# Optimization experiments

Measured on AMD Instinct MI355X. Metric: run time of the kernel, lower is better.

## Reference

```python
import jax, jax.numpy as jnp
import numpy as np

NEG_INF = -1.0e9  # matches torch code's masked fill value


def setup_inputs() -> dict:
    key = jax.random.key(0)
    k1, k2, k3, k4 = jax.random.split(key, 4)
    n, q, s, d, v = 8, 4096, 4096, 64, 64
    return {
        "queries_nqd": jax.random.normal(k1, (n, q, d), dtype=jnp.float32),
        "keys_nsd": jax.random.normal(k2, (n, s, d), dtype=jnp.float32),
        "values_nsv": jax.random.normal(k3, (n, s, v), dtype=jnp.float32),
        "attention_mask_nqs": jax.random.randint(k4, (n, q, s), 0, 2).astype(jnp.bool_),
    }


def reference(queries_nqd, keys_nsd, values_nsv, attention_mask_nqs):
    d = queries_nqd.shape[-1]
    scale = 1.0 / jnp.sqrt(jnp.asarray(d, dtype=queries_nqd.dtype))
    # [n,q,s] = [n,q,d] @ [n,d,s]
    scores_nqs = jnp.einsum("nqd,nsd->nqs", queries_nqd, keys_nsd) * scale
    scores_nqs = jnp.where(attention_mask_nqs, scores_nqs, jnp.asarray(NEG_INF, scores_nqs.dtype))
    probs_nqs = jax.nn.softmax(scores_nqs, axis=-1)
    # dropout p=0.0 (eval) -> identity
    return jnp.einsum("nqs,nsv->nqv", probs_nqs, values_nsv)
```

## Files before the change

kernel.cpp:

```cpp
#include <hip/hip_runtime.h>
#include <hip/hip_bf16.h>


#define NHEADS 8
#define QLEN   4096
#define SLEN   4096
#define DDIM   64
#define VDIM   64
#define SBLK   64
#define QBLK   64
#define NWAVES 4
#define NCHUNK (SLEN / SBLK)

typedef __bf16          bf16x4 __attribute__((ext_vector_type(4)));
typedef __bf16          bf16x8 __attribute__((ext_vector_type(8)));
typedef float           f32x4  __attribute__((ext_vector_type(4)));
typedef unsigned int    u32x4  __attribute__((ext_vector_type(4)));
typedef unsigned short  u16x4  __attribute__((ext_vector_type(4)));

#define KSWZ(s) (((s) & 7) << 4)
#define VSWZ(v) ((((v) >> 2) & 7) << 4)

__device__ __forceinline__ int detect_mfmt(const unsigned char* __restrict__ M) {
  const int lane = threadIdx.x & 63;
  u32x4 w = *((const u32x4*)M + lane);
  unsigned o = w[0] | w[1] | w[2] | w[3];
  unsigned comb = ((o & 0x00FFFF00u) ? 1u : 0u) | ((o & 0x000000FFu) ? 2u : 0u);
  comb |= __shfl_xor((int)comb, 1);  comb |= __shfl_xor((int)comb, 2);
  comb |= __shfl_xor((int)comb, 4);  comb |= __shfl_xor((int)comb, 8);
  comb |= __shfl_xor((int)comb, 16); comb |= __shfl_xor((int)comb, 32);
  return ((comb & 1u) == 0u) ? 1 : (((comb & 2u) == 0u) ? 2 : 0);
}

struct MaskRegs {
  unsigned w8[4];
  u32x4    w32[4];
};

__global__ __launch_bounds__(256, 2)
void attn_fwd_kernel(const float* __restrict__ Qg, const float* __restrict__ Kg,
                     const float* __restrict__ Vg, const unsigned char* __restrict__ Mg,
                     float* __restrict__ Og)
{
  __shared__ __align__(16) unsigned short Ksh[2][64 * 64];
  __shared__ __align__(16) unsigned short Vsh[2][64 * 64];
  __shared__ __align__(16) unsigned short Psh[NWAVES][16 * 64];

  const int mfmt = detect_mfmt(Mg);

  const int tid  = threadIdx.x;
  const int wave = tid >> 6;
  const int lane = tid & 63;
  const int g    = lane >> 4;
  const int lq   = lane & 15;

  const int head = blockIdx.x;
  const int qblk = blockIdx.y;

  const float* Qp = Qg + ((size_t)head * QLEN + (size_t)qblk * QBLK) * DDIM;
  const float* Kp = Kg + (size_t)head * SLEN * DDIM;
  const float* Vp = Vg + (size_t)head * SLEN * VDIM;
  float* Op = Og + ((size_t)head * QLEN + (size_t)qblk * QBLK) * DDIM;

  const float QSCALE = 0.125f * 1.44269504f;
  const int qrow = wave * 16 + lq;
  bf16x8 qf[2];
#pragma unroll
  for (int ks = 0; ks < 2; ++ks) {
    const float* qp = Qp + (size_t)qrow * DDIM + 8 * g + 32 * ks;
    f32x4 a = *(const f32x4*)qp;
    f32x4 b = *(const f32x4*)(qp + 4);
    bf16x8 t;
#pragma unroll
    for (int j = 0; j < 4; ++j) { t[j] = (__bf16)(a[j] * QSCALE); t[4 + j] = (__bf16)(b[j] * QSCALE); }
    qf[ks] = t;
  }

  const size_t mrow_elems = ((size_t)head * QLEN + (size_t)qblk * QBLK + qrow) * SLEN;
  const unsigned char* mrow8  = Mg + mrow_elems;
  const unsigned*      mrow32 = (const unsigned*)Mg + mrow_elems;

  f32x4 oacc[4];
#pragma unroll
  for (int vt = 0; vt < 4; ++vt) oacc[vt] = (f32x4){0.f, 0.f, 0.f, 0.f};
  float m_run = -INFINITY;
  float l_run = 0.f;

#define PREFETCH_KV(S0)                                                        \
  _Pragma("unroll")                                                            \
  for (int it = 0; it < 4; ++it) {                                             \
    int srow = (tid >> 4) + it * 16;                                           \
    int d0   = (tid & 15) * 4;                                                 \
    kpre[it] = *(const f32x4*)(Kp + (size_t)((S0) + srow) * DDIM + d0);        \
    vpre[it] = *(const f32x4*)(Vp + (size_t)((S0) + srow) * VDIM + d0);        \
  }

#define WRITE_KV(BUF)                                                          \
  _Pragma("unroll")                                                            \
  for (int it = 0; it < 4; ++it) {                                             \
    int srow = (tid >> 4) + it * 16;                                           \
    int d0   = (tid & 15) * 4;                                                 \
    bf16x4 kb;                                                                 \
    _Pragma("unroll") for (int j = 0; j < 4; ++j) kb[j] = (__bf16)kpre[it][j]; \
    int koff = (srow * 128 + d0 * 2) ^ KSWZ(srow);                             \
    *(u16x4*)((char*)Ksh[BUF] + koff) = __builtin_bit_cast(u16x4, kb);         \
    _Pragma("unroll")                                                          \
    for (int j = 0; j < 4; ++j) {                                              \
      int v = d0 + j;                                                          \
      unsigned short b = __builtin_bit_cast(unsigned short, (__bf16)vpre[it][j]); \
      int voff = (v * 128 + srow * 2) ^ VSWZ(v);                               \
      *(unsigned short*)((char*)Vsh[BUF] + voff) = b;                          \
    }                                                                          \
  }

#define LOAD_MASK(MR, S0)                                                      \
  if (mfmt == 0) {                                                             \
    _Pragma("unroll")                                                          \
    for (int st = 0; st < 4; ++st)                                             \
      MR.w8[st] = *(const unsigned*)(mrow8 + (S0) + 16 * st + 4 * g);          \
  } else {                                                                     \
    _Pragma("unroll")                                                          \
    for (int st = 0; st < 4; ++st)                                             \
      MR.w32[st] = *(const u32x4*)(mrow32 + (S0) + 16 * st + 4 * g);           \
  }

#define CHUNK_BODY(C, CUR, MUSE, MLOAD) {                                      \
  const bool hasn = ((C) + 1 < NCHUNK);                                        \
  f32x4 kpre[4]; f32x4 vpre[4];                                                \
  if (hasn) {                                                                  \
    const int s0n = ((C) + 1) * SBLK;                                          \
    PREFETCH_KV(s0n);                                                          \
    LOAD_MASK(MLOAD, s0n);                                                     \
  }                                                                            \
                               \
  f32x4 sacc[4];                                                               \
  _Pragma("unroll")                                                            \
  for (int st = 0; st < 4; ++st) sacc[st] = (f32x4){0.f, 0.f, 0.f, 0.f};       \
  _Pragma("unroll")                                                            \
  for (int st = 0; st < 4; ++st) {                                             \
    int srow = lq + 16 * st;                                                   \
    _Pragma("unroll")                                                          \
    for (int ks = 0; ks < 2; ++ks) {                                           \
      int off = (srow * 128 + (8 * g + 32 * ks) * 2) ^ KSWZ(srow);             \
      bf16x8 kf = *(const bf16x8*)((const char*)Ksh[CUR] + off);               \
      sacc[st] = __builtin_amdgcn_mfma_f32_16x16x32_bf16(kf, qf[ks], sacc[st], 0, 0, 0); \
    }                                                                          \
  }                                                                            \
                      \
  float vals[4][4];                                                            \
  float mloc = -INFINITY;                                                      \
  _Pragma("unroll")                                                            \
  for (int st = 0; st < 4; ++st) {                                             \
    bool keep[4];                                                              \
    if (mfmt == 0) {                                                           \
      _Pragma("unroll")                                                        \
      for (int r = 0; r < 4; ++r) keep[r] = ((MUSE.w8[st] >> (8 * r)) & 0xFFu) != 0u; \
    } else {                                                                   \
      _Pragma("unroll")                                                        \
      for (int r = 0; r < 4; ++r) keep[r] = MUSE.w32[st][r] != 0u;             \
    }                                                                          \
    _Pragma("unroll")                                                          \
    for (int r = 0; r < 4; ++r) {                                              \
      float v = keep[r] ? sacc[st][r] : -1.0e9f;                               \
      vals[st][r] = v;                                                         \
      mloc = fmaxf(mloc, v);                                                   \
    }                                                                          \
  }                                                                            \
  mloc = fmaxf(mloc, __shfl_xor(mloc, 16));                                    \
  mloc = fmaxf(mloc, __shfl_xor(mloc, 32));                                    \
  float m_new = fmaxf(m_run, mloc);                                            \
  float alpha = __builtin_amdgcn_exp2f(m_run - m_new);                         \
  float lsum = 0.f;                                                            \
  _Pragma("unroll")                                                            \
  for (int st = 0; st < 4; ++st) {                                             \
    bf16x4 pb;                                                                 \
    _Pragma("unroll")                                                          \
    for (int r = 0; r < 4; ++r) {                                              \
      float p = __builtin_amdgcn_exp2f(vals[st][r] - m_new);                   \
      lsum += p;                                                               \
      pb[r] = (__bf16)p;                                                       \
    }                                                                          \
    int off = (lq * 128 + (16 * st + 4 * g) * 2) ^ KSWZ(lq);                   \
    *(u16x4*)((char*)Psh[wave] + off) = __builtin_bit_cast(u16x4, pb);         \
  }                                                                            \
  lsum += __shfl_xor(lsum, 16);                                                \
  lsum += __shfl_xor(lsum, 32);                                                \
  l_run = l_run * alpha + lsum;                                                \
  m_run = m_new;                                                               \
  _Pragma("unroll")                                                            \
  for (int vt = 0; vt < 4; ++vt) {                                             \
    _Pragma("unroll")                                                          \
    for (int r = 0; r < 4; ++r) oacc[vt][r] *= alpha;                          \
  }                                                                            \
                                                \
  _Pragma("unroll")                                                            \
  for (int ks = 0; ks < 2; ++ks) {                                             \
    int poff = (lq * 128 + (8 * g + 32 * ks) * 2) ^ KSWZ(lq);                  \
    bf16x8 pf = *(const bf16x8*)((const char*)Psh[wave] + poff);               \
    _Pragma("unroll")                                                          \
    for (int vt = 0; vt < 4; ++vt) {                                           \
      int vrow = lq + 16 * vt;                                                 \
      int voff = (vrow * 128 + (8 * g + 32 * ks) * 2) ^ VSWZ(vrow);            \
      bf16x8 vf = *(const bf16x8*)((const char*)Vsh[CUR] + voff);              \
      oacc[vt] = __builtin_amdgcn_mfma_f32_16x16x32_bf16(vf, pf, oacc[vt], 0, 0, 0); \
    }                                                                          \
  }                                                                            \
  if (hasn) { WRITE_KV((CUR) ^ 1); }                                           \
  __syncthreads();                                                             \
}

  MaskRegs mA, mB;

  {
    f32x4 kpre[4]; f32x4 vpre[4];
    PREFETCH_KV(0);
    LOAD_MASK(mA, 0);
    WRITE_KV(0);
    __syncthreads();
  }

  for (int cc = 0; cc < NCHUNK; cc += 2) {
    CHUNK_BODY(cc,     0, mA, mB);
    CHUNK_BODY(cc + 1, 1, mB, mA);
  }

  float inv_l = 1.0f / l_run;
  float* orow = Op + (size_t)qrow * VDIM;
#pragma unroll
  for (int vt = 0; vt < 4; ++vt) {
    f32x4 o;
#pragma unroll
    for (int r = 0; r < 4; ++r) o[r] = oacc[vt][r] * inv_l;
    *(f32x4*)(orow + 16 * vt + 4 * g) = o;
  }
}

extern "C" void kernel_launch(void* const* d_in, const int* in_sizes, int n_in,
                              void* d_out, int out_size, void* d_ws, size_t ws_size,
                              hipStream_t stream) {
  const float* Qg = (const float*)d_in[0];
  const float* Kg = (const float*)d_in[1];
  const float* Vg = (const float*)d_in[2];
  const unsigned char* Mg = (const unsigned char*)d_in[3];
  float* Og = (float*)d_out;

  dim3 grid(NHEADS, QLEN / QBLK);
  dim3 block(256);
  attn_fwd_kernel<<<grid, block, 0, stream>>>(Qg, Kg, Vg, Mg, Og);
}
```

Measured before the change: 155.2 us.

## Split key range across two wave groups, template mask format, lazy rescale

```diff
diff --git a/kernel.cpp b/kernel.cpp
--- a/kernel.cpp
+++ b/kernel.cpp
@@ -9,8 +9,8 @@
 #define VDIM   64
 #define SBLK   64
 #define QBLK   64
-#define NWAVES 4
-#define NCHUNK (SLEN / SBLK)
+#define NSTEP  32
+#define QSTRIDE 20
 
 typedef __bf16          bf16x4 __attribute__((ext_vector_type(4)));
 typedef __bf16          bf16x8 __attribute__((ext_vector_type(8)));
@@ -32,38 +32,40 @@
   return ((comb & 1u) == 0u) ? 1 : (((comb & 2u) == 0u) ? 2 : 0);
 }
 
-struct MaskRegs {
-  unsigned w8[4];
-  u32x4    w32[4];
-};
-
-__global__ __launch_bounds__(256, 2)
-void attn_fwd_kernel(const float* __restrict__ Qg, const float* __restrict__ Kg,
-                     const float* __restrict__ Vg, const unsigned char* __restrict__ Mg,
-                     float* __restrict__ Og)
+template<bool U8>
+__global__ __launch_bounds__(512, 4)
+void attn_fwd(const float* __restrict__ Qg, const float* __restrict__ Kg,
+              const float* __restrict__ Vg, const unsigned char* __restrict__ Mg,
+              float* __restrict__ Og)
 {
-  __shared__ __align__(16) unsigned short Ksh[2][64 * 64];
-  __shared__ __align__(16) unsigned short Vsh[2][64 * 64];
-  __shared__ __align__(16) unsigned short Psh[NWAVES][16 * 64];
-
-  const int mfmt = detect_mfmt(Mg);
+  __shared__ __align__(16) unsigned short Ksh[2][2][64 * 64];
+  __shared__ __align__(16) unsigned short Vsh[2][2][64 * 64];
+  __shared__ __align__(16) unsigned short Psh[8][16 * 64];
+
+  {
+    const int mfmt = detect_mfmt(Mg);
+    if (U8 ? (mfmt != 0) : (mfmt == 0)) return;
+  }
 
   const int tid  = threadIdx.x;
   const int wave = tid >> 6;
   const int lane = tid & 63;
   const int g    = lane >> 4;
   const int lq   = lane & 15;
+  const int half = wave >> 2;
+  const int wq   = wave & 3;
+  const int hid  = tid & 255;
 
   const int head = blockIdx.x;
   const int qblk = blockIdx.y;
 
   const float* Qp = Qg + ((size_t)head * QLEN + (size_t)qblk * QBLK) * DDIM;
-  const float* Kp = Kg + (size_t)head * SLEN * DDIM;
-  const float* Vp = Vg + (size_t)head * SLEN * VDIM;
+  const float* Kp = Kg + (size_t)head * SLEN * DDIM + (size_t)half * NSTEP * SBLK * DDIM;
+  const float* Vp = Vg + (size_t)head * SLEN * VDIM + (size_t)half * NSTEP * SBLK * VDIM;
   float* Op = Og + ((size_t)head * QLEN + (size_t)qblk * QBLK) * DDIM;
 
   const float QSCALE = 0.125f * 1.44269504f;
-  const int qrow = wave * 16 + lq;
+  const int qrow = wq * 16 + lq;
   bf16x8 qf[2];
 #pragma unroll
   for (int ks = 0; ks < 2; ++ks) {
@@ -76,9 +78,9 @@
     qf[ks] = t;
   }
 
-  const size_t mrow_elems = ((size_t)head * QLEN + (size_t)qblk * QBLK + qrow) * SLEN;
-  const unsigned char* mrow8  = Mg + mrow_elems;
-  const unsigned*      mrow32 = (const unsigned*)Mg + mrow_elems;
+  const size_t mbase = ((size_t)head * QLEN + (size_t)qblk * QBLK + qrow) * SLEN;
+  const unsigned char* mrow8  = Mg + mbase + (size_t)half * NSTEP * SBLK;
+  const unsigned*      mrow32 = (const unsigned*)Mg + mbase + (size_t)half * NSTEP * SBLK;
 
   f32x4 oacc[4];
 #pragma unroll
@@ -86,78 +88,82 @@
   float m_run = -INFINITY;
   float l_run = 0.f;
 
-#define PREFETCH_KV(S0)                                                        \
+  unsigned m8A[4],  m8B[4];
+  u32x4    m32A[4], m32B[4];
+
+#define PREFETCH_KV(STEPN)                                                     \
   _Pragma("unroll")                                                            \
   for (int it = 0; it < 4; ++it) {                                             \
-    int srow = (tid >> 4) + it * 16;                                           \
-    int d0   = (tid & 15) * 4;                                                 \
-    kpre[it] = *(const f32x4*)(Kp + (size_t)((S0) + srow) * DDIM + d0);        \
-    vpre[it] = *(const f32x4*)(Vp + (size_t)((S0) + srow) * VDIM + d0);        \
+    int srow = (hid >> 4) + it * 16;                                           \
+    int d0   = (hid & 15) * 4;                                                 \
+    kpre[it] = *(const f32x4*)(Kp + (size_t)((STEPN) * SBLK + srow) * DDIM + d0); \
+    vpre[it] = *(const f32x4*)(Vp + (size_t)((STEPN) * SBLK + srow) * VDIM + d0); \
   }
 
 #define WRITE_KV(BUF)                                                          \
   _Pragma("unroll")                                                            \
   for (int it = 0; it < 4; ++it) {                                             \
-    int srow = (tid >> 4) + it * 16;                                           \
-    int d0   = (tid & 15) * 4;                                                 \
+    int srow = (hid >> 4) + it * 16;                                           \
+    int d0   = (hid & 15) * 4;                                                 \
     bf16x4 kb;                                                                 \
     _Pragma("unroll") for (int j = 0; j < 4; ++j) kb[j] = (__bf16)kpre[it][j]; \
     int koff = (srow * 128 + d0 * 2) ^ KSWZ(srow);                             \
-    *(u16x4*)((char*)Ksh[BUF] + koff) = __builtin_bit_cast(u16x4, kb);         \
+    *(u16x4*)((char*)Ksh[half][BUF] + koff) = __builtin_bit_cast(u16x4, kb);   \
     _Pragma("unroll")                                                          \
     for (int j = 0; j < 4; ++j) {                                              \
       int v = d0 + j;                                                          \
       unsigned short b = __builtin_bit_cast(unsigned short, (__bf16)vpre[it][j]); \
       int voff = (v * 128 + srow * 2) ^ VSWZ(v);                               \
-      *(unsigned short*)((char*)Vsh[BUF] + voff) = b;                          \
-    }                                                                          \
-  }
-
-#define LOAD_MASK(MR, S0)                                                      \
-  if (mfmt == 0) {                                                             \
+      *(unsigned short*)((char*)Vsh[half][BUF] + voff) = b;                    \
+    }                                                                          \
+  }
+
+#define LOAD_MASK(M8, M32, S0)                                                 \
+  if constexpr (U8) {                                                          \
     _Pragma("unroll")                                                          \
     for (int st = 0; st < 4; ++st)                                             \
-      MR.w8[st] = *(const unsigned*)(mrow8 + (S0) + 16 * st + 4 * g);          \
+      M8[st] = *(const unsigned*)(mrow8 + (S0) + 16 * st + 4 * g);             \
   } else {                                                                     \
     _Pragma("unroll")                                                          \
     for (int st = 0; st < 4; ++st)                                             \
-      MR.w32[st] = *(const u32x4*)(mrow32 + (S0) + 16 * st + 4 * g);           \
-  }
-
-#define CHUNK_BODY(C, CUR, MUSE, MLOAD) {                                      \
-  const bool hasn = ((C) + 1 < NCHUNK);                                        \
+      M32[st] = *(const u32x4*)(mrow32 + (S0) + 16 * st + 4 * g);              \
+  }
+
+#define CHUNK_BODY(STEP, CUR, MU8, MU32, ML8, ML32) {                          \
+  const bool hasn = ((STEP) + 1 < NSTEP);                                      \
   f32x4 kpre[4]; f32x4 vpre[4];                                                \
   if (hasn) {                                                                  \
-    const int s0n = ((C) + 1) * SBLK;                                          \
-    PREFETCH_KV(s0n);                                                          \
-    LOAD_MASK(MLOAD, s0n);                                                     \
+    PREFETCH_KV((STEP) + 1);                                                   \
+    LOAD_MASK(ML8, ML32, ((STEP) + 1) * SBLK);                                 \
   }                                                                            \
                                \
   f32x4 sacc[4];                                                               \
   _Pragma("unroll")                                                            \
   for (int st = 0; st < 4; ++st) sacc[st] = (f32x4){0.f, 0.f, 0.f, 0.f};       \
+  __builtin_amdgcn_s_setprio(1);                                               \
   _Pragma("unroll")                                                            \
   for (int st = 0; st < 4; ++st) {                                             \
     int srow = lq + 16 * st;                                                   \
     _Pragma("unroll")                                                          \
     for (int ks = 0; ks < 2; ++ks) {                                           \
       int off = (srow * 128 + (8 * g + 32 * ks) * 2) ^ KSWZ(srow);             \
-      bf16x8 kf = *(const bf16x8*)((const char*)Ksh[CUR] + off);               \
+      bf16x8 kf = *(const bf16x8*)((const char*)Ksh[half][CUR] + off);         \
       sacc[st] = __builtin_amdgcn_mfma_f32_16x16x32_bf16(kf, qf[ks], sacc[st], 0, 0, 0); \
     }                                                                          \
   }                                                                            \
+  __builtin_amdgcn_s_setprio(0);                                               \
                       \
   float vals[4][4];                                                            \
   float mloc = -INFINITY;                                                      \
   _Pragma("unroll")                                                            \
   for (int st = 0; st < 4; ++st) {                                             \
     bool keep[4];                                                              \
-    if (mfmt == 0) {                                                           \
+    if constexpr (U8) {                                                        \
       _Pragma("unroll")                                                        \
-      for (int r = 0; r < 4; ++r) keep[r] = ((MUSE.w8[st] >> (8 * r)) & 0xFFu) != 0u; \
+      for (int r = 0; r < 4; ++r) keep[r] = ((MU8[st] >> (8 * r)) & 0xFFu) != 0u; \
     } else {                                                                   \
       _Pragma("unroll")                                                        \
-      for (int r = 0; r < 4; ++r) keep[r] = MUSE.w32[st][r] != 0u;             \
+      for (int r = 0; r < 4; ++r) keep[r] = MU32[st][r] != 0u;                 \
     }                                                                          \
     _Pragma("unroll")                                                          \
     for (int r = 0; r < 4; ++r) {                                              \
@@ -168,15 +174,25 @@
   }                                                                            \
   mloc = fmaxf(mloc, __shfl_xor(mloc, 16));                                    \
   mloc = fmaxf(mloc, __shfl_xor(mloc, 32));                                    \
-  float m_new = fmaxf(m_run, mloc);                                            \
-  float alpha = __builtin_amdgcn_exp2f(m_run - m_new);                         \
+      \
+  if (!__all(mloc <= m_run + 8.0f)) {                                          \
+    float m_new = fmaxf(m_run, mloc);                                          \
+    float alpha = __builtin_amdgcn_exp2f(m_run - m_new);                       \
+    l_run *= alpha;                                                            \
+    _Pragma("unroll")                                                          \
+    for (int vt = 0; vt < 4; ++vt) {                                           \
+      _Pragma("unroll")                                                        \
+      for (int r = 0; r < 4; ++r) oacc[vt][r] *= alpha;                        \
+    }                                                                          \
+    m_run = m_new;                                                             \
+  }                                                                            \
   float lsum = 0.f;                                                            \
   _Pragma("unroll")                                                            \
   for (int st = 0; st < 4; ++st) {                                             \
     bf16x4 pb;                                                                 \
     _Pragma("unroll")                                                          \
     for (int r = 0; r < 4; ++r) {                                              \
-      float p = __builtin_amdgcn_exp2f(vals[st][r] - m_new);                   \
+      float p = __builtin_amdgcn_exp2f(vals[st][r] - m_run);                   \
       lsum += p;                                                               \
       pb[r] = (__bf16)p;                                                       \
     }                                                                          \
@@ -185,14 +201,9 @@
   }                                                                            \
   lsum += __shfl_xor(lsum, 16);                                                \
   lsum += __shfl_xor(lsum, 32);                                                \
-  l_run = l_run * alpha + lsum;                                                \
-  m_run = m_new;                                                               \
-  _Pragma("unroll")                                                            \
-  for (int vt = 0; vt < 4; ++vt) {                                             \
-    _Pragma("unroll")                                                          \
-    for (int r = 0; r < 4; ++r) oacc[vt][r] *= alpha;                          \
-  }                                                                            \
+  l_run += lsum;                                                               \
                                                 \
+  __builtin_amdgcn_s_setprio(1);                                               \
   _Pragma("unroll")                                                            \
   for (int ks = 0; ks < 2; ++ks) {                                             \
     int poff = (lq * 128 + (8 * g + 32 * ks) * 2) ^ KSWZ(lq);                  \
@@ -201,38 +212,67 @@
     for (int vt = 0; vt < 4; ++vt) {                                           \
       int vrow = lq + 16 * vt;                                                 \
       int voff = (vrow * 128 + (8 * g + 32 * ks) * 2) ^ VSWZ(vrow);            \
-      bf16x8 vf = *(const bf16x8*)((const char*)Vsh[CUR] + voff);              \
+      bf16x8 vf = *(const bf16x8*)((const char*)Vsh[half][CUR] + voff);        \
       oacc[vt] = __builtin_amdgcn_mfma_f32_16x16x32_bf16(vf, pf, oacc[vt], 0, 0, 0); \
     }                                                                          \
   }                                                                            \
+  __builtin_amdgcn_s_setprio(0);                                               \
   if (hasn) { WRITE_KV((CUR) ^ 1); }                                           \
   __syncthreads();                                                             \
 }
-
-  MaskRegs mA, mB;
 
   {
     f32x4 kpre[4]; f32x4 vpre[4];
     PREFETCH_KV(0);
-    LOAD_MASK(mA, 0);
+    LOAD_MASK(m8A, m32A, 0);
     WRITE_KV(0);
     __syncthreads();
   }
 
-  for (int cc = 0; cc < NCHUNK; cc += 2) {
-    CHUNK_BODY(cc,     0, mA, mB);
-    CHUNK_BODY(cc + 1, 1, mB, mA);
-  }
-
-  float inv_l = 1.0f / l_run;
-  float* orow = Op + (size_t)qrow * VDIM;
-#pragma unroll
-  for (int vt = 0; vt < 4; ++vt) {
-    f32x4 o;
-#pragma unroll
-    for (int r = 0; r < 4; ++r) o[r] = oacc[vt][r] * inv_l;
-    *(f32x4*)(orow + 16 * vt + 4 * g) = o;
-  }
+  for (int ss = 0; ss < NSTEP; ss += 2) {
+    CHUNK_BODY(ss,     0, m8A, m32A, m8B, m32B);
+    CHUNK_BODY(ss + 1, 1, m8B, m32B, m8A, m32A);
+  }
+
+  float* mO = (float*)&Ksh[0][0][0];
+  float* mM = (float*)&Vsh[0][0][0];
+  __syncthreads();
+  if (half == 1) {
+#pragma unroll
+    for (int vt = 0; vt < 4; ++vt) {
+#pragma unroll
+      for (int r = 0; r < 4; ++r)
+        mO[((size_t)wq * 64 + 16 * vt + 4 * g + r) * QSTRIDE + lq] = oacc[vt][r];
+    }
+    if (g == 0) {
+      mM[(wq * 2 + 0) * 16 + lq] = m_run;
+      mM[(wq * 2 + 1) * 16 + lq] = l_run;
+    }
+  }
+  __syncthreads();
+  if (half == 0) {
+    float m1 = mM[(wq * 2 + 0) * 16 + lq];
+    float l1 = mM[(wq * 2 + 1) * 16 + lq];
+    float mm = fmaxf(m_run, m1);
+    float a0 = __builtin_amdgcn_exp2f(m_run - mm);
+    float a1 = __builtin_amdgcn_exp2f(m1 - mm);
+    float inv = 1.0f / (l_run * a0 + l1 * a1);
+    float* orow = Op + (size_t)qrow * VDIM;
+#pragma unroll
+    for (int vt = 0; vt < 4; ++vt) {
+      f32x4 o;
+#pragma unroll
+      for (int r = 0; r < 4; ++r) {
+        float o1 = mO[((size_t)wq * 64 + 16 * vt + 4 * g + r) * QSTRIDE + lq];
+        o[r] = (oacc[vt][r] * a0 + o1 * a1) * inv;
+      }
+      *(f32x4*)(orow + 16 * vt + 4 * g) = o;
+    }
+  }
+#undef PREFETCH_KV
+#undef WRITE_KV
+#undef LOAD_MASK
+#undef CHUNK_BODY
 }
 
 extern "C" void kernel_launch(void* const* d_in, const int* in_sizes, int n_in,
@@ -245,6 +285,7 @@
   float* Og = (float*)d_out;
 
   dim3 grid(NHEADS, QLEN / QBLK);
-  dim3 block(256);
-  attn_fwd_kernel<<<grid, block, 0, stream>>>(Qg, Kg, Vg, Mg, Og);
-}
+  dim3 block(512);
+  attn_fwd<true ><<<grid, block, 0, stream>>>(Qg, Kg, Vg, Mg, Og);
+  attn_fwd<false><<<grid, block, 0, stream>>>(Qg, Kg, Vg, Mg, Og);
+}
```

Result: slower. 573.7 us (+269.7%).
